# Performance work log

Hardware: AMD Instinct MI355X
Metric: run time of the kernel (lower is better)

Reference implementation:

```python
import jax, jax.numpy as jnp
import numpy as np

EXPERT_ID = 3
NUM_EXPERTS = 8
FULL_DIM = 4096
EXPERT_DIM = 1024
SLICE = FULL_DIM // NUM_EXPERTS          # 512
S0 = EXPERT_ID * SLICE
S1 = S0 + SLICE
FP_MIN = EXPERT_ID / NUM_EXPERTS         # 0.375
FP_MAX = (EXPERT_ID + 1) / NUM_EXPERTS   # 0.5
GATE_HID = SLICE // 4                    # 128


def _xavier(key, shape):
    fan_out, fan_in = shape
    lim = float(np.sqrt(6.0 / (fan_in + fan_out)))
    return jax.random.uniform(key, shape, minval=-lim, maxval=lim, dtype=jnp.float32)


def setup_inputs() -> dict:
    key = jax.random.key(0)
    ks = jax.random.split(key, 9)
    B, P = 4, 4096
    tokens = jax.random.normal(ks[0], (B, P, FULL_DIM), dtype=jnp.float32)
    fingerprints = jax.random.uniform(ks[1], (P,), dtype=jnp.float32)
    # learned params (torch nn.Linear stores weight as [out, in])
    gate_w1 = _xavier(ks[2], (GATE_HID, SLICE))
    gate_b1 = jnp.zeros((GATE_HID,), dtype=jnp.float32)
    gate_w2 = _xavier(ks[3], (1, GATE_HID))
    gate_b2 = jnp.zeros((1,), dtype=jnp.float32)
    wq = _xavier(ks[4], (EXPERT_DIM, SLICE))
    wk = _xavier(ks[5], (EXPERT_DIM, SLICE))
    wv = _xavier(ks[6], (EXPERT_DIM, SLICE))
    penta = jax.random.normal(ks[7], (5, EXPERT_DIM), dtype=jnp.float32) * 0.02
    penta = penta / jnp.linalg.norm(penta, axis=-1, keepdims=True)  # _init_weights normalizes
    alpha = jnp.asarray(1.0, dtype=jnp.float32)
    return {
        'tokens': tokens, 'fingerprints': fingerprints, 'alpha': alpha,
        'gate_w1': gate_w1, 'gate_b1': gate_b1, 'gate_w2': gate_w2, 'gate_b2': gate_b2,
        'wq': wq, 'wk': wk, 'wv': wv, 'pentachoron': penta,
    }


def reference(tokens, fingerprints, alpha, gate_w1, gate_b1, gate_w2, gate_b2,
              wq, wk, wv, pentachoron):
    # expert 3 is not the last expert -> strict upper bound
    mask = (fingerprints >= FP_MIN) & (fingerprints < FP_MAX)        # [P] bool
    # gather selected patches, then slice this expert's feature band
    my_features = tokens[..., S0:S1][:, mask]                        # [B, p, SLICE]
    # gating MLP: Linear -> GELU(exact) -> Linear -> Sigmoid
    h = jax.nn.gelu(my_features @ gate_w1.T + gate_b1, approximate=False)
    alpha_gate = jax.nn.sigmoid(h @ gate_w2.T + gate_b2)             # [B, p, 1]
    alpha_weight = jax.nn.sigmoid(alpha)
    my_features = my_features * (alpha_gate * alpha_weight + (1.0 - alpha_weight))
    Q = my_features @ wq.T                                           # [B, p, D]
    K = my_features @ wk.T
    V = my_features @ wv.T
    # per-vertex affinities, vectorized over the 5 pentachoron vertices
    dirs = pentachoron / jnp.linalg.norm(pentachoron, axis=-1, keepdims=True)
    K_aff = jnp.einsum('bpd,vd->vbp', K, dirs)                       # [5, B, p]
    Q_aff = jnp.einsum('bpd,vd->vbp', Q, dirs)
    return (Q, K, V, K_aff, Q_aff, mask)
```

## Files before the change

kernel.cpp:

```cpp
#include <hip/hip_runtime.h>
#include <hip/hip_bf16.h>

#define FULL_DIM 4096
#define EXPERT_DIM 1024
#define SLICE 512
#define S0 (3*SLICE)
#define GATE_HID 128
#define P_TOK 4096
#define BATCH 4
#define NCONV 1536
#define NCW 16

typedef __bf16 bf16;
typedef __bf16 bf16x4 __attribute__((ext_vector_type(4)));
typedef __bf16 bf16x8 __attribute__((ext_vector_type(8)));
typedef float f32x4 __attribute__((ext_vector_type(4)));

__device__ inline void gl_lds16(const void* g, void* l) {
    __builtin_amdgcn_global_load_lds((const __attribute__((address_space(1))) void*)g,
                                     (__attribute__((address_space(3))) void*)l, 16, 0, 0);
}

__launch_bounds__(256)
__global__ void k_front(const float* __restrict__ tokens, const float* __restrict__ fp,
                        const float* __restrict__ alpha,
                        const float* __restrict__ gw1, const float* __restrict__ gb1,
                        const float* __restrict__ gw2, const float* __restrict__ gb2,
                        const float* __restrict__ wq, const float* __restrict__ wk,
                        const float* __restrict__ wv, const float* __restrict__ penta,
                        bf16* __restrict__ wqkvb, float* __restrict__ cwp,
                        float* __restrict__ mask_out, bf16* __restrict__ Fs,
                        int p, int M, int ngate) {
    __shared__ bf16 F[32][520];
    __shared__ union { bf16 W1[128][72]; float H[32][132]; } u;
    __shared__ int trow[32];
    __shared__ float scl[32];
    __shared__ int sOffs[256];
    __shared__ unsigned short sBits[256];
    __shared__ int wsum[4];
    __shared__ float sd[5][64];
    __shared__ float red[5][4];
    const int bid = blockIdx.x, t = threadIdx.x;
    const int wave = t >> 6, lane = t & 63;

    if (bid < ngate) {
        const int fr = lane & 15, fq = lane >> 4;
        const int m0 = bid * 32;
        {
            int base = t * 16;
            unsigned bits = 0;
            int cnt = 0;
#pragma unroll
            for (int i = 0; i < 16; i++) {
                float v = fp[base + i];
                bool m = (v >= 0.375f) && (v < 0.5f);
                bits |= ((unsigned)m) << i;
                cnt += (int)m;
            }
            int incl = cnt;
#pragma unroll
            for (int d = 1; d < 64; d <<= 1) {
                int n = __shfl_up(incl, d);
                if (lane >= d) incl += n;
            }
            if (lane == 63) wsum[wave] = incl;
            __syncthreads();
            int wbase = 0;
            for (int w = 0; w < 4; w++) if (w < wave) wbase += wsum[w];
            sOffs[t] = wbase + incl - cnt;
            sBits[t] = (unsigned short)bits;
        }
        __syncthreads();
        if (t < 32) {
            int m = m0 + t;
            int r = -1;
            if (m < M) {
                int b = m / p, j = m - b * p;
                int lo = 0, hi = 255;
                while (lo < hi) { int mid = (lo + hi + 1) >> 1; if (sOffs[mid] <= j) lo = mid; else hi = mid - 1; }
                int jj = j - sOffs[lo];
                unsigned bt = sBits[lo];
                int pos = 0;
#pragma unroll
                for (int bit = 0; bit < 16; bit++) {
                    if ((bt >> bit) & 1) { if (jj == 0) { pos = bit; break; } jj--; }
                }
                r = b * P_TOK + lo * 16 + pos;
            }
            trow[t] = r;
        }
        __syncthreads();
#pragma unroll
        for (int it = 0; it < 16; it++) {
            int r = it * 2 + (t >> 7);
            int c4 = (t & 127) * 4;
            int tr = trow[r];
            float4 v = {0.f, 0.f, 0.f, 0.f};
            if (tr >= 0) v = *(const float4*)(tokens + (size_t)tr * FULL_DIM + S0 + c4);
            bf16x4 b = { (bf16)v.x, (bf16)v.y, (bf16)v.z, (bf16)v.w };
            *(bf16x4*)(&F[r][c4]) = b;
        }
        __syncthreads();
        f32x4 acc[2][2];
#pragma unroll
        for (int i = 0; i < 2; i++)
#pragma unroll
            for (int j = 0; j < 2; j++) acc[i][j] = (f32x4){0.f, 0.f, 0.f, 0.f};
        for (int k0 = 0; k0 < 512; k0 += 64) {
            {
                int n = t >> 1, ch = (t & 1) * 32;
                const float* src = gw1 + (size_t)n * 512 + k0 + ch;
#pragma unroll
                for (int q = 0; q < 4; q++) {
                    float4 a = *(const float4*)(src + q * 8);
                    float4 b = *(const float4*)(src + q * 8 + 4);
                    bf16x8 w = { (bf16)a.x, (bf16)a.y, (bf16)a.z, (bf16)a.w,
                                 (bf16)b.x, (bf16)b.y, (bf16)b.z, (bf16)b.w };
                    *(bf16x8*)(&u.W1[n][ch + q * 8]) = w;
                }
            }
            __syncthreads();
#pragma unroll
            for (int ks = 0; ks < 2; ks++) {
                bf16x8 a0 = *(const bf16x8*)(&F[fr][k0 + ks * 32 + fq * 8]);
                bf16x8 a1 = *(const bf16x8*)(&F[16 + fr][k0 + ks * 32 + fq * 8]);
                bf16x8 b0 = *(const bf16x8*)(&u.W1[wave * 32 + fr][ks * 32 + fq * 8]);
                bf16x8 b1 = *(const bf16x8*)(&u.W1[wave * 32 + 16 + fr][ks * 32 + fq * 8]);
                acc[0][0] = __builtin_amdgcn_mfma_f32_16x16x32_bf16(a0, b0, acc[0][0], 0, 0, 0);
                acc[0][1] = __builtin_amdgcn_mfma_f32_16x16x32_bf16(a0, b1, acc[0][1], 0, 0, 0);
                acc[1][0] = __builtin_amdgcn_mfma_f32_16x16x32_bf16(a1, b0, acc[1][0], 0, 0, 0);
                acc[1][1] = __builtin_amdgcn_mfma_f32_16x16x32_bf16(a1, b1, acc[1][1], 0, 0, 0);
            }
            __syncthreads();
        }
#pragma unroll
        for (int mi = 0; mi < 2; mi++)
#pragma unroll
            for (int ni = 0; ni < 2; ni++) {
                int col = wave * 32 + ni * 16 + fr;
                float bias = gb1[col];
#pragma unroll
                for (int r = 0; r < 4; r++) {
                    int row = mi * 16 + fq * 4 + r;
                    float v = acc[mi][ni][r] + bias;
                    u.H[row][col] = 0.5f * v * (1.0f + erff(v * 0.70710678118f));
                }
            }
        __syncthreads();
        {
            int r = wave * 8 + (lane >> 3), g = lane & 7;
            float s = 0.f;
#pragma unroll
            for (int i = 0; i < 16; i++) { int c = g + i * 8; s += u.H[r][c] * gw2[c]; }
            s += __shfl_xor(s, 1); s += __shfl_xor(s, 2); s += __shfl_xor(s, 4);
            if (g == 0) {
                float aw = 1.0f / (1.0f + expf(-alpha[0]));
                float gt = 1.0f / (1.0f + expf(-(s + gb2[0])));
                scl[r] = gt * aw + (1.0f - aw);
            }
        }
        __syncthreads();
#pragma unroll
        for (int it = 0; it < 16; it++) {
            int r = it * 2 + (t >> 7);
            int c4 = (t & 127) * 4;
            bf16x4 b = *(const bf16x4*)(&F[r][c4]);
            float sc = scl[r];
            bf16x4 o = { (bf16)((float)b[0] * sc), (bf16)((float)b[1] * sc),
                         (bf16)((float)b[2] * sc), (bf16)((float)b[3] * sc) };
            *(bf16x4*)(Fs + (size_t)(m0 + r) * 512 + c4) = o;
        }
        return;
    }
    if (bid == ngate) {
        int base = t * 16;
#pragma unroll
        for (int i = 0; i < 16; i++) {
            float v = fp[base + i];
            mask_out[base + i] = ((v >= 0.375f) && (v < 0.5f)) ? 1.0f : 0.0f;
        }
        return;
    }
    if (bid <= ngate + NCW) {
        const int cb = bid - (ngate + 1);
        const int d0 = cb * 64;
#pragma unroll
        for (int v = 0; v < 5; v++) {
            float s = 0.f;
#pragma unroll
            for (int i = 0; i < 4; i++) { float x = penta[v * 1024 + t + i * 256]; s += x * x; }
            for (int d = 32; d; d >>= 1) s += __shfl_xor(s, d);
            if (lane == 0) red[v][wave] = s;
        }
        __syncthreads();
        for (int e = t; e < 5 * 64; e += 256) {
            int v = e >> 6, dd = e & 63;
            float inv = rsqrtf(red[v][0] + red[v][1] + red[v][2] + red[v][3]);
            sd[v][dd] = penta[v * 1024 + d0 + dd] * inv;
        }
        __syncthreads();
#pragma unroll
        for (int pass = 0; pass < 2; pass++) {
            int col = pass * 256 + t;
            float aK[5] = {0, 0, 0, 0, 0}, aQ[5] = {0, 0, 0, 0, 0};
            for (int d = 0; d < 64; d += 4) {
#pragma unroll
                for (int uu = 0; uu < 4; uu++) {
                    float kv = wk[(size_t)(d0 + d + uu) * 512 + col];
                    float qv = wq[(size_t)(d0 + d + uu) * 512 + col];
#pragma unroll
                    for (int v = 0; v < 5; v++) {
                        float dv = sd[v][d + uu];
                        aK[v] += dv * kv;
                        aQ[v] += dv * qv;
                    }
                }
            }
#pragma unroll
            for (int v = 0; v < 5; v++) {
                cwp[((size_t)cb * 10 + v) * 512 + col] = aK[v];
                cwp[((size_t)cb * 10 + 5 + v) * 512 + col] = aQ[v];
            }
        }
        return;
    }
    {
        int ci = bid - (ngate + 1 + NCW);
        int i = ci * 1024 + t * 4;
        const float* src = (i < 524288) ? wq : (i < 2 * 524288 ? wk : wv);
        float4 v = *(const float4*)(src + (i & 524287));
        bf16x4 b = { (bf16)v.x, (bf16)v.y, (bf16)v.z, (bf16)v.w };
        *(bf16x4*)(wqkvb + i) = b;
    }
}

__launch_bounds__(512)
__global__ void k_qkv(const bf16* __restrict__ A, const bf16* __restrict__ W,
                      const float* __restrict__ cwp, float* __restrict__ out,
                      float* __restrict__ aff, int M) {
    __shared__ bf16 As[2][256 * 32];
    __shared__ bf16 Bs[2][128 * 32];
    const int t = threadIdx.x, wave = t >> 6, lane = t & 63;
    const int fr = lane & 15, fq = lane >> 4;

    if (blockIdx.y == 24) {
        bf16* cwt = (bf16*)As;
        for (int e = t; e < 16 * 512; e += 512) {
            int v = e >> 9, c = e & 511;
            float s = 0.f;
            if (v < 10) {
#pragma unroll
                for (int cb = 0; cb < NCW; cb++)
                    s += cwp[((size_t)cb * 10 + v) * 512 + c];
            }
            int byte = v * 1024 + ((((c >> 3) ^ (v & 7)) << 4)) + (c & 7) * 2;
            *(bf16*)((char*)cwt + byte) = (bf16)s;
        }
        __syncthreads();
        const int m0w = blockIdx.x * 256 + wave * 32;
        f32x4 acc0 = (f32x4){0.f, 0.f, 0.f, 0.f};
        f32x4 acc1 = (f32x4){0.f, 0.f, 0.f, 0.f};
        for (int k0 = 0; k0 < 512; k0 += 32) {
            int chunk = (k0 >> 3) + fq;
            bf16x8 b = *(const bf16x8*)((char*)cwt + fr * 1024 + ((chunk ^ (fr & 7)) << 4));
            bf16x8 a0 = *(const bf16x8*)(A + (size_t)(m0w + fr) * 512 + k0 + fq * 8);
            bf16x8 a1 = *(const bf16x8*)(A + (size_t)(m0w + 16 + fr) * 512 + k0 + fq * 8);
            acc0 = __builtin_amdgcn_mfma_f32_16x16x32_bf16(a0, b, acc0, 0, 0, 0);
            acc1 = __builtin_amdgcn_mfma_f32_16x16x32_bf16(a1, b, acc1, 0, 0, 0);
        }
        if (fr < 10) {
#pragma unroll
            for (int r = 0; r < 4; r++) {
                int m = m0w + fq * 4 + r;
                if (m < M) aff[(size_t)fr * M + m] = acc0[r];
                m += 16;
                if (m < M) aff[(size_t)fr * M + m] = acc1[r];
            }
        }
        return;
    }

    const int m0 = blockIdx.x * 256, n0 = blockIdx.y * 128;
    const int wr = wave >> 1, wc = wave & 1;

    f32x4 acc[4][4];
#pragma unroll
    for (int i = 0; i < 4; i++)
#pragma unroll
        for (int j = 0; j < 4; j++) acc[i][j] = (f32x4){0.f, 0.f, 0.f, 0.f};

    const bf16* ga = A + (size_t)(m0 + (t >> 2)) * 512 + (t & 3) * 8;
    const bf16* gb = W + (size_t)(n0 + (t >> 2)) * 512 + (t & 3) * 8;

#define STAGE(buf, ko)                                               \
    gl_lds16(ga + (ko),             &As[buf][wave * 512]);           \
    gl_lds16(ga + (ko) + 128 * 512, &As[buf][4096 + wave * 512]);    \
    gl_lds16(gb + (ko),             &Bs[buf][wave * 512]);

    STAGE(0, 0);
    __syncthreads();
    int cur = 0;
    for (int kt = 0; kt < 16; kt++) {
        if (kt < 15) { STAGE(cur ^ 1, (kt + 1) * 32); }
        bf16x8 af[4], bw[4];
#pragma unroll
        for (int mi = 0; mi < 4; mi++)
            af[mi] = *(const bf16x8*)(&As[cur][(wr * 64 + mi * 16 + fr) * 32 + fq * 8]);
#pragma unroll
        for (int ni = 0; ni < 4; ni++)
            bw[ni] = *(const bf16x8*)(&Bs[cur][(wc * 64 + ni * 16 + fr) * 32 + fq * 8]);
#pragma unroll
        for (int mi = 0; mi < 4; mi++)
#pragma unroll
            for (int ni = 0; ni < 4; ni++)
                acc[mi][ni] = __builtin_amdgcn_mfma_f32_16x16x32_bf16(af[mi], bw[ni], acc[mi][ni], 0, 0, 0);
        __syncthreads();
        cur ^= 1;
    }
#undef STAGE

    const int z = blockIdx.y >> 3;
    const int nb = (blockIdx.y & 7) * 128;
    float* obase = out + (size_t)z * M * EXPERT_DIM;
#pragma unroll
    for (int mi = 0; mi < 4; mi++)
#pragma unroll
        for (int ni = 0; ni < 4; ni++) {
            int col = nb + wc * 64 + ni * 16 + fr;
#pragma unroll
            for (int r = 0; r < 4; r++) {
                int row = m0 + wr * 64 + mi * 16 + fq * 4 + r;
                if (row < M) obase[(size_t)row * EXPERT_DIM + col] = acc[mi][ni][r];
            }
        }
}

extern "C" void kernel_launch(void* const* d_in, const int* in_sizes, int n_in,
                              void* d_out, int out_size, void* d_ws, size_t ws_size,
                              hipStream_t stream) {
    const float* tokens = (const float*)d_in[0];
    const float* fps    = (const float*)d_in[1];
    const float* alpha  = (const float*)d_in[2];
    const float* gw1    = (const float*)d_in[3];
    const float* gb1    = (const float*)d_in[4];
    const float* gw2    = (const float*)d_in[5];
    const float* gb2    = (const float*)d_in[6];
    const float* wq     = (const float*)d_in[7];
    const float* wk     = (const float*)d_in[8];
    const float* wv     = (const float*)d_in[9];
    const float* penta  = (const float*)d_in[10];
    float* out = (float*)d_out;

    int p = (out_size - P_TOK) / (3 * BATCH * EXPERT_DIM + 2 * 5 * BATCH);
    if (p <= 0) return;
    int M = BATCH * p;
    int Mpad = (M + 255) & ~255;
    int ngate = Mpad / 32;

    char* ws = (char*)d_ws;
    size_t off = 0;
    bf16*  wqkvb = (bf16*)(ws + off);  off += (size_t)3 * EXPERT_DIM * SLICE * 2;
    float* cwp   = (float*)(ws + off); off += (size_t)NCW * 10 * 512 * 4;
    bf16*  Fs    = (bf16*)(ws + off);  off += (size_t)Mpad * SLICE * 2;
    (void)ws_size;

    float* aff_out  = out + (size_t)3 * M * EXPERT_DIM;
    float* mask_out = aff_out + (size_t)10 * M;

    k_front<<<ngate + 1 + NCW + NCONV, 256, 0, stream>>>(
        tokens, fps, alpha, gw1, gb1, gw2, gb2, wq, wk, wv, penta,
        wqkvb, cwp, mask_out, Fs, p, M, ngate);
    k_qkv<<<dim3(Mpad / 256, 25), 512, 0, stream>>>(Fs, wqkvb, cwp, out, aff_out, M);
}
```

Measured before the change: 49.59 us.

## Triple-buffer QKV GEMM LDS staging with explicit vmcnt waits

After: 49.61 us. No clear change (+0.0%).

```diff
diff --git a/kernel.cpp b/kernel.cpp
--- a/kernel.cpp
+++ b/kernel.cpp
@@ -238,8 +238,8 @@
 __global__ void k_qkv(const bf16* __restrict__ A, const bf16* __restrict__ W,
                       const float* __restrict__ cwp, float* __restrict__ out,
                       float* __restrict__ aff, int M) {
-    __shared__ bf16 As[2][256 * 32];
-    __shared__ bf16 Bs[2][128 * 32];
+    __shared__ bf16 As[3][256 * 32];
+    __shared__ bf16 Bs[3][128 * 32];
     const int t = threadIdx.x, wave = t >> 6, lane = t & 63;
     const int fr = lane & 15, fq = lane >> 4;
 
@@ -297,27 +297,44 @@
     gl_lds16(ga + (ko) + 128 * 512, &As[buf][4096 + wave * 512]);    \
     gl_lds16(gb + (ko),             &Bs[buf][wave * 512]);
 
+#define COMPUTE(buf)                                                                     \
+    {                                                                                    \
+        bf16x8 af[4], bw[4];                                                             \
+        _Pragma("unroll")                                                                \
+        for (int mi = 0; mi < 4; mi++)                                                   \
+            af[mi] = *(const bf16x8*)(&As[buf][(wr * 64 + mi * 16 + fr) * 32 + fq * 8]); \
+        _Pragma("unroll")                                                                \
+        for (int ni = 0; ni < 4; ni++)                                                   \
+            bw[ni] = *(const bf16x8*)(&Bs[buf][(wc * 64 + ni * 16 + fr) * 32 + fq * 8]); \
+        _Pragma("unroll")                                                                \
+        for (int mi = 0; mi < 4; mi++)                                                   \
+            _Pragma("unroll")                                                            \
+            for (int ni = 0; ni < 4; ni++)                                               \
+                acc[mi][ni] = __builtin_amdgcn_mfma_f32_16x16x32_bf16(af[mi], bw[ni], acc[mi][ni], 0, 0, 0); \
+    }
+
     STAGE(0, 0);
-    __syncthreads();
-    int cur = 0;
-    for (int kt = 0; kt < 16; kt++) {
-        if (kt < 15) { STAGE(cur ^ 1, (kt + 1) * 32); }
-        bf16x8 af[4], bw[4];
-#pragma unroll
-        for (int mi = 0; mi < 4; mi++)
-            af[mi] = *(const bf16x8*)(&As[cur][(wr * 64 + mi * 16 + fr) * 32 + fq * 8]);
-#pragma unroll
-        for (int ni = 0; ni < 4; ni++)
-            bw[ni] = *(const bf16x8*)(&Bs[cur][(wc * 64 + ni * 16 + fr) * 32 + fq * 8]);
-#pragma unroll
-        for (int mi = 0; mi < 4; mi++)
-#pragma unroll
-            for (int ni = 0; ni < 4; ni++)
-                acc[mi][ni] = __builtin_amdgcn_mfma_f32_16x16x32_bf16(af[mi], bw[ni], acc[mi][ni], 0, 0, 0);
-        __syncthreads();
-        cur ^= 1;
-    }
+    STAGE(1, 32);
+    int cur = 0, pre = 2;
+#pragma unroll 1
+    for (int kt = 0; kt < 14; kt++) {
+        STAGE(pre, (kt + 2) * 32);
+        asm volatile("s_waitcnt vmcnt(6)" ::: "memory");
+        __builtin_amdgcn_s_barrier();
+        COMPUTE(cur);
+        __builtin_amdgcn_s_barrier();
+        cur = (cur == 2) ? 0 : cur + 1;
+        pre = (pre == 2) ? 0 : pre + 1;
+    }
+    asm volatile("s_waitcnt vmcnt(3)" ::: "memory");
+    __builtin_amdgcn_s_barrier();
+    COMPUTE(cur);
+    cur = (cur == 2) ? 0 : cur + 1;
+    asm volatile("s_waitcnt vmcnt(0)" ::: "memory");
+    __builtin_amdgcn_s_barrier();
+    COMPUTE(cur);
 #undef STAGE
+#undef COMPUTE
 
     const int z = blockIdx.y >> 3;
     const int nb = (blockIdx.y & 7) * 128;
```

## Double K-tile depth to 64 with XOR-swizzled LDS and explicit vmcnt waits

Applied to the files above, without the earlier changes.

New measurement: 49.81 us. No clear change (+0.5%).

```diff
diff --git a/kernel.cpp b/kernel.cpp
--- a/kernel.cpp
+++ b/kernel.cpp
@@ -238,8 +238,8 @@
 __global__ void k_qkv(const bf16* __restrict__ A, const bf16* __restrict__ W,
                       const float* __restrict__ cwp, float* __restrict__ out,
                       float* __restrict__ aff, int M) {
-    __shared__ bf16 As[2][256 * 32];
-    __shared__ bf16 Bs[2][128 * 32];
+    __shared__ bf16 As[2][256 * 64];
+    __shared__ bf16 Bs[2][128 * 64];
     const int t = threadIdx.x, wave = t >> 6, lane = t & 63;
     const int fr = lane & 15, fq = lane >> 4;
 
@@ -289,35 +289,55 @@
 #pragma unroll
         for (int j = 0; j < 4; j++) acc[i][j] = (f32x4){0.f, 0.f, 0.f, 0.f};
 
-    const bf16* ga = A + (size_t)(m0 + (t >> 2)) * 512 + (t & 3) * 8;
-    const bf16* gb = W + (size_t)(n0 + (t >> 2)) * 512 + (t & 3) * 8;
-
-#define STAGE(buf, ko)                                               \
-    gl_lds16(ga + (ko),             &As[buf][wave * 512]);           \
-    gl_lds16(ga + (ko) + 128 * 512, &As[buf][4096 + wave * 512]);    \
-    gl_lds16(gb + (ko),             &Bs[buf][wave * 512]);
+    const int lr = lane >> 3;
+    const int js = (lane & 7) ^ lr;
+    const bf16* gaL = A + (size_t)(m0 + wave * 32 + lr) * 512 + js * 8;
+    const bf16* gbL = W + (size_t)(n0 + wave * 16 + lr) * 512 + js * 8;
+    const int xr = fr & 7;
+
+#define STAGE(buf, ko)                                                \
+    gl_lds16(gaL + (ko),            &As[buf][(wave * 4 + 0) * 512]);  \
+    gl_lds16(gaL + (ko) +  8 * 512, &As[buf][(wave * 4 + 1) * 512]);  \
+    gl_lds16(gaL + (ko) + 16 * 512, &As[buf][(wave * 4 + 2) * 512]);  \
+    gl_lds16(gaL + (ko) + 24 * 512, &As[buf][(wave * 4 + 3) * 512]);  \
+    gl_lds16(gbL + (ko),            &Bs[buf][(wave * 2 + 0) * 512]);  \
+    gl_lds16(gbL + (ko) +  8 * 512, &Bs[buf][(wave * 2 + 1) * 512]);
+
+#define COMPUTE(buf)                                                                      \
+    _Pragma("unroll")                                                                     \
+    for (int ks = 0; ks < 2; ks++) {                                                      \
+        const int co = ((ks * 4 + fq) ^ xr) * 8;                                          \
+        bf16x8 af[4], bw[4];                                                              \
+        _Pragma("unroll")                                                                 \
+        for (int mi = 0; mi < 4; mi++)                                                    \
+            af[mi] = *(const bf16x8*)(&As[buf][(wr * 64 + mi * 16 + fr) * 64 + co]);      \
+        _Pragma("unroll")                                                                 \
+        for (int ni = 0; ni < 4; ni++)                                                    \
+            bw[ni] = *(const bf16x8*)(&Bs[buf][(wc * 64 + ni * 16 + fr) * 64 + co]);      \
+        _Pragma("unroll")                                                                 \
+        for (int mi = 0; mi < 4; mi++)                                                    \
+            _Pragma("unroll")                                                             \
+            for (int ni = 0; ni < 4; ni++)                                                \
+                acc[mi][ni] = __builtin_amdgcn_mfma_f32_16x16x32_bf16(af[mi], bw[ni], acc[mi][ni], 0, 0, 0); \
+    }
 
     STAGE(0, 0);
-    __syncthreads();
     int cur = 0;
-    for (int kt = 0; kt < 16; kt++) {
-        if (kt < 15) { STAGE(cur ^ 1, (kt + 1) * 32); }
-        bf16x8 af[4], bw[4];
-#pragma unroll
-        for (int mi = 0; mi < 4; mi++)
-            af[mi] = *(const bf16x8*)(&As[cur][(wr * 64 + mi * 16 + fr) * 32 + fq * 8]);
-#pragma unroll
-        for (int ni = 0; ni < 4; ni++)
-            bw[ni] = *(const bf16x8*)(&Bs[cur][(wc * 64 + ni * 16 + fr) * 32 + fq * 8]);
-#pragma unroll
-        for (int mi = 0; mi < 4; mi++)
-#pragma unroll
-            for (int ni = 0; ni < 4; ni++)
-                acc[mi][ni] = __builtin_amdgcn_mfma_f32_16x16x32_bf16(af[mi], bw[ni], acc[mi][ni], 0, 0, 0);
-        __syncthreads();
+#pragma unroll 1
+    for (int kt = 0; kt < 8; kt++) {
+        if (kt < 7) {
+            STAGE(cur ^ 1, (kt + 1) * 64);
+            asm volatile("s_waitcnt vmcnt(6)" ::: "memory");
+        } else {
+            asm volatile("s_waitcnt vmcnt(0)" ::: "memory");
+        }
+        __builtin_amdgcn_s_barrier();
+        COMPUTE(cur);
+        __builtin_amdgcn_s_barrier();
         cur ^= 1;
     }
 #undef STAGE
+#undef COMPUTE
 
     const int z = blockIdx.y >> 3;
     const int nb = (blockIdx.y & 7) * 128;
```
